# Kernel tuning notes

Hardware: AMD Instinct MI355X
Metric: run time of the kernel (lower is better)

## Reference

```python
import jax, jax.numpy as jnp
import numpy as np

HEAD = 12  # number of attention heads (init kwarg)


def setup_inputs() -> dict:
    key = jax.random.key(0)
    ks = jax.random.split(key, 6)
    B, N, F = 16, 1024, 768
    return {
        "x": jax.random.normal(ks[0], (B, N, F), dtype=jnp.float32),
        "wq": jax.random.normal(ks[1], (F,), dtype=jnp.float32),
        "bq": jnp.zeros((F,), dtype=jnp.float32),
        "wk": jax.random.normal(ks[2], (F,), dtype=jnp.float32),
        "bk": jnp.zeros((F,), dtype=jnp.float32),
        "wv": jax.random.normal(ks[3], (F,), dtype=jnp.float32),
        "bv": jnp.zeros((F,), dtype=jnp.float32),
        "wo": jax.random.normal(ks[4], (F,), dtype=jnp.float32),
        "bo": jnp.zeros((F,), dtype=jnp.float32),
    }


def reference(x, wq, bq, wk, bk, wv, bv, wo, bo):
    # x: [B, N, F]; depthwise (per-channel) q/k/v projections, MHSA, depthwise out proj
    B, N, F = x.shape
    d = F // HEAD
    scale = jnp.asarray(F, x.dtype) ** 0.5  # repo uses sqrt(feats), not sqrt(d_head)

    def to_heads(t):
        return t.reshape(B, N, HEAD, d)

    q = to_heads(x * wq + bq)  # [B, N, H, d]
    k = to_heads(x * wk + bk)
    v = to_heads(x * wv + bv)

    att = jnp.einsum("bqhd,bkhd->bhqk", q, k) / scale  # [B, H, N, N]
    att = jax.nn.softmax(att, axis=-1)
    o = jnp.einsum("bhqk,bkhd->bqhd", att, v).reshape(B, N, F)
    return o * wo + bo
```

## Files before the change

### kernel.cpp

```cpp
#include <hip/hip_runtime.h>
#include <hip/hip_bf16.h>
#include <cstdint>
#include <cstddef>

typedef __attribute__((ext_vector_type(8))) short short8;
typedef __attribute__((ext_vector_type(4))) short short4v;
typedef __attribute__((ext_vector_type(4))) float f32x4;
typedef __attribute__((ext_vector_type(16))) float f32x16;
typedef __attribute__((ext_vector_type(4))) unsigned int uint4v;

static constexpr int B_ = 16, N_ = 1024, F_ = 768, H_ = 12, D_ = 64;
static constexpr int NB = 64, NT = N_ / NB;
static constexpr int QB = 128;
static constexpr float RSCALE = 0.036084391824351615f;
static constexpr float QSCALE = 0.036084391824351615f * 1.4426950408889634f;
static constexpr float DEFER_THR = 8.0f;

__device__ __forceinline__ short f2bf(float f) {
    return __builtin_bit_cast(short, __float2bfloat16(f));
}
__device__ __forceinline__ unsigned cvtpk(float lo, float hi) {
    unsigned r;
    asm("v_cvt_pk_bf16_f32 %0, %1, %2" : "=v"(r) : "v"(lo), "v"(hi));
    return r;
}

#define GLB(p)  ((const __attribute__((address_space(1))) void*)(p))
#define LDSP(p) ((__attribute__((address_space(3))) void*)(p))

__global__ void __launch_bounds__(256) prep_kv(
    const float* __restrict__ x,
    const float* __restrict__ wk, const float* __restrict__ bk,
    const float* __restrict__ wv, const float* __restrict__ bv,
    short* __restrict__ Kt, short* __restrict__ Vt)
{
    const int bid = blockIdx.x;
    const int t   = bid & 15;
    const int bh  = bid >> 4;
    const int h   = bh % H_, b = bh / H_;
    const int nb  = t * NB;
    const int tid = threadIdx.x;
    short* Ktile = Kt + ((size_t)bid << 12);
    short* Vtile = Vt + ((size_t)bid << 12);

    {
        const int n = tid >> 2, sg = tid & 3;
        const float* xr  = x  + ((size_t)(b * N_ + nb + n)) * F_ + h * D_ + sg * 16;
        const float* wkp = wk + h * D_ + sg * 16;
        const float* bkp = bk + h * D_ + sg * 16;
        float xv[16];
        #pragma unroll
        for (int q = 0; q < 4; ++q) *(float4*)&xv[q * 4] = *(const float4*)(xr + q * 4);
        short kb[16];
        #pragma unroll
        for (int i = 0; i < 16; ++i) kb[i] = f2bf(xv[i] * wkp[i] + bkp[i]);
        const int swz = n & 7;
        #pragma unroll
        for (int c2 = 0; c2 < 2; ++c2) {
            const int c = sg * 2 + c2;
            *(short8*)&Ktile[n * 64 + ((c ^ swz) << 3)] = *(short8*)&kb[c2 * 8];
        }
    }
    {
        const int d = tid & 63, ng = tid >> 6;
        const float wvd = wv[h * D_ + d], bvd = bv[h * D_ + d];
        const float* xc = x + ((size_t)(b * N_ + nb + ng * 16)) * F_ + h * D_ + d;
        short vb[16];
        #pragma unroll
        for (int j = 0; j < 16; ++j) vb[j] = f2bf(xc[(size_t)j * F_] * wvd + bvd);
        const int swz = d & 7;
        #pragma unroll
        for (int c2 = 0; c2 < 2; ++c2) {
            const int c = ng * 2 + c2;
            *(short8*)&Vtile[d * 64 + ((c ^ swz) << 3)] = *(short8*)&vb[c2 * 8];
        }
    }
}

__global__ void __launch_bounds__(256, 4) attn_main(
    const float* __restrict__ x,
    const float* __restrict__ wq, const float* __restrict__ bq,
    const short* __restrict__ Kt, const short* __restrict__ Vt,
    const float* __restrict__ wo, const float* __restrict__ bo,
    float* __restrict__ out)
{
    __shared__ short KV[2][2][4096];

    const int tid  = threadIdx.x;
    const int w    = tid >> 6, lane = tid & 63;
    const int q32  = lane & 31, hi = lane >> 5;

    const int orig = blockIdx.x;
    const int sb   = (orig & 7) * 192 + (orig >> 3);
    const int qt   = sb & 7, bh = sb >> 3;
    const int h    = bh % H_, b = bh / H_;
    const int qrow0 = qt * QB + w * 32;
    const int qa    = qrow0 + q32;

    short8 qf[4];
    {
        const float* xq = x + ((size_t)(b * N_ + qa)) * F_ + h * D_;
        #pragma unroll
        for (int s = 0; s < 4; ++s) {
            const int ch0 = s * 16 + hi * 8;
            float4 a0 = *(const float4*)(xq + ch0);
            float4 a1 = *(const float4*)(xq + ch0 + 4);
            const float* wqp = wq + h * D_ + ch0;
            const float* bqp = bq + h * D_ + ch0;
            float q8[8] = {a0.x,a0.y,a0.z,a0.w,a1.x,a1.y,a1.z,a1.w};
            uint4v u;
            #pragma unroll
            for (int j = 0; j < 4; ++j) {
                const float lo = (q8[2*j]   * wqp[2*j]   + bqp[2*j])   * QSCALE;
                const float hf = (q8[2*j+1] * wqp[2*j+1] + bqp[2*j+1]) * QSCALE;
                u[j] = cvtpk(lo, hf);
            }
            qf[s] = __builtin_bit_cast(short8, u);
        }
    }

    const int swz = q32 & 7;
    int coff[4];
    #pragma unroll
    for (int s = 0; s < 4; ++s) coff[s] = (((s * 2 + hi) ^ swz) << 3);
    const int rA = q32 * 64;
    const int rB = (32 + q32) * 64;

    float m_ = 0.f, l_ = 0.f;
    f32x16 oA, oB;
    #pragma unroll
    for (int r = 0; r < 16; ++r) { oA[r] = 0.f; oB[r] = 0.f; }

    const size_t base = ((size_t)bh) * (NT * 4096);
    auto stage = [&](int buf, int tt) {
        const short* tk = Kt + base + ((size_t)tt << 12) + w * 1024 + (lane << 3);
        const short* tv = Vt + base + ((size_t)tt << 12) + w * 1024 + (lane << 3);
        __builtin_amdgcn_global_load_lds(GLB(tk),       LDSP(&KV[buf][0][w*1024]),       16, 0, 0);
        __builtin_amdgcn_global_load_lds(GLB(tk + 512), LDSP(&KV[buf][0][w*1024 + 512]), 16, 0, 0);
        __builtin_amdgcn_global_load_lds(GLB(tv),       LDSP(&KV[buf][1][w*1024]),       16, 0, 0);
        __builtin_amdgcn_global_load_lds(GLB(tv + 512), LDSP(&KV[buf][1][w*1024 + 512]), 16, 0, 0);
    };

    stage(0, 0);

    for (int t = 0; t < NT; ++t) {
        const int cur = t & 1;
        __syncthreads();
        if (t + 1 < NT) stage(cur ^ 1, t + 1);
        const short* Kb = &KV[cur][0][0];
        const short* Vb = &KV[cur][1][0];

        const float negm = -m_;
        f32x16 sA, sB;
        #pragma unroll
        for (int r = 0; r < 16; ++r) { sA[r] = negm; sB[r] = negm; }
        __builtin_amdgcn_s_setprio(1);
        #pragma unroll
        for (int s = 0; s < 4; ++s) {
            short8 k0 = *(const short8*)&Kb[rA + coff[s]];
            short8 k1 = *(const short8*)&Kb[rB + coff[s]];
            sA = __builtin_amdgcn_mfma_f32_32x32x16_bf16(k0, qf[s], sA, 0, 0, 0);
            sB = __builtin_amdgcn_mfma_f32_32x32x16_bf16(k1, qf[s], sB, 0, 0, 0);
        }
        __builtin_amdgcn_s_setprio(0);

        float mx[16];
        #pragma unroll
        for (int r = 0; r < 16; ++r) mx[r] = fmaxf(sA[r], sB[r]);
        #pragma unroll
        for (int off = 8; off > 0; off >>= 1) {
            #pragma unroll
            for (int i = 0; i < 8; ++i)
                if (i < off) mx[i] = fmaxf(mx[i], mx[i + off]);
        }
        const float tm = fmaxf(mx[0], __shfl_xor(mx[0], 32, 64));

        if (!__all(tm <= DEFER_THR)) {
            const float corr = __builtin_amdgcn_exp2f(-tm);
            l_ *= corr;
            #pragma unroll
            for (int r = 0; r < 16; ++r) { oA[r] *= corr; oB[r] *= corr; }
            #pragma unroll
            for (int r = 0; r < 16; ++r) { sA[r] -= tm; sB[r] -= tm; }
            m_ += tm;
        }

        float e[32];
        #pragma unroll
        for (int r = 0; r < 16; ++r) {
            e[r]      = __builtin_amdgcn_exp2f(sA[r]);
            e[16 + r] = __builtin_amdgcn_exp2f(sB[r]);
        }
        float su[16];
        #pragma unroll
        for (int i = 0; i < 16; ++i) su[i] = e[i] + e[i + 16];
        #pragma unroll
        for (int off = 8; off > 0; off >>= 1) {
            #pragma unroll
            for (int i = 0; i < 8; ++i)
                if (i < off) su[i] += su[i + off];
        }
        l_ += su[0] + __shfl_xor(su[0], 32, 64);

        short8 pf[4];
        {
            uint4v u0, u1, u2, u3;
            u0[0] = cvtpk(e[0],  e[1]);  u0[1] = cvtpk(e[2],  e[3]);
            u0[2] = cvtpk(e[4],  e[5]);  u0[3] = cvtpk(e[6],  e[7]);
            u1[0] = cvtpk(e[8],  e[9]);  u1[1] = cvtpk(e[10], e[11]);
            u1[2] = cvtpk(e[12], e[13]); u1[3] = cvtpk(e[14], e[15]);
            u2[0] = cvtpk(e[16], e[17]); u2[1] = cvtpk(e[18], e[19]);
            u2[2] = cvtpk(e[20], e[21]); u2[3] = cvtpk(e[22], e[23]);
            u3[0] = cvtpk(e[24], e[25]); u3[1] = cvtpk(e[26], e[27]);
            u3[2] = cvtpk(e[28], e[29]); u3[3] = cvtpk(e[30], e[31]);
            pf[0] = __builtin_bit_cast(short8, u0);
            pf[1] = __builtin_bit_cast(short8, u1);
            pf[2] = __builtin_bit_cast(short8, u2);
            pf[3] = __builtin_bit_cast(short8, u3);
        }

        __builtin_amdgcn_s_setprio(1);
        #pragma unroll
        for (int s = 0; s < 4; ++s) {
            const int cLo = ((2*s    ) ^ swz) << 3;
            const int cHi = ((2*s + 1) ^ swz) << 3;
            short4v aLo = *(const short4v*)&Vb[rA + cLo + 4*hi];
            short4v aHi = *(const short4v*)&Vb[rA + cHi + 4*hi];
            short4v bLo = *(const short4v*)&Vb[rB + cLo + 4*hi];
            short4v bHi = *(const short4v*)&Vb[rB + cHi + 4*hi];
            short8 v0 = {aLo[0],aLo[1],aLo[2],aLo[3], aHi[0],aHi[1],aHi[2],aHi[3]};
            short8 v1 = {bLo[0],bLo[1],bLo[2],bLo[3], bHi[0],bHi[1],bHi[2],bHi[3]};
            oA = __builtin_amdgcn_mfma_f32_32x32x16_bf16(v0, pf[s], oA, 0, 0, 0);
            oB = __builtin_amdgcn_mfma_f32_32x32x16_bf16(v1, pf[s], oB, 0, 0, 0);
        }
        __builtin_amdgcn_s_setprio(0);
    }

    const float invl = 1.f / l_;
    float* orow = out + ((size_t)(b * N_ + qa)) * F_;
    #pragma unroll
    for (int dsb = 0; dsb < 2; ++dsb) {
        #pragma unroll
        for (int j = 0; j < 4; ++j) {
            const int ch = h * D_ + dsb * 32 + 8 * j + 4 * hi;
            float4 wv = *(const float4*)(wo + ch);
            float4 bv = *(const float4*)(bo + ch);
            float4 o4;
            if (dsb == 0) {
                o4.x = oA[4*j+0] * invl * wv.x + bv.x;
                o4.y = oA[4*j+1] * invl * wv.y + bv.y;
                o4.z = oA[4*j+2] * invl * wv.z + bv.z;
                o4.w = oA[4*j+3] * invl * wv.w + bv.w;
            } else {
                o4.x = oB[4*j+0] * invl * wv.x + bv.x;
                o4.y = oB[4*j+1] * invl * wv.y + bv.y;
                o4.z = oB[4*j+2] * invl * wv.z + bv.z;
                o4.w = oB[4*j+3] * invl * wv.w + bv.w;
            }
            *(float4*)(orow + ch) = o4;
        }
    }
}

__global__ void __launch_bounds__(256) attn_fused(
    const float* __restrict__ x,
    const float* __restrict__ wq, const float* __restrict__ bq,
    const float* __restrict__ wk, const float* __restrict__ bk,
    const float* __restrict__ wv, const float* __restrict__ bv,
    const float* __restrict__ wo, const float* __restrict__ bo,
    float* __restrict__ out)
{
    __shared__ short Klds[64][72];
    __shared__ short Vt[64][72];
    __shared__ short Plds[4][16][72];

    const int tid = threadIdx.x;
    const int wave = tid >> 6, lane = tid & 63;
    const int g = lane >> 4, cc = lane & 15;
    const int bid = blockIdx.x;
    const int qt = bid & 15, t1 = bid >> 4;
    const int h = t1 % H_, b = t1 / H_;

    const int qrow = qt * 64 + wave * 16 + cc;
    const float* xq = x + ((size_t)(b * N_ + qrow)) * F_ + h * D_;
    short8 qf[2];
    #pragma unroll
    for (int kc = 0; kc < 2; ++kc) {
        const int dd = kc * 32 + g * 8;
        float4 a0 = *(const float4*)(xq + dd);
        float4 a1 = *(const float4*)(xq + dd + 4);
        float qa[8] = {a0.x,a0.y,a0.z,a0.w,a1.x,a1.y,a1.z,a1.w};
        #pragma unroll
        for (int i = 0; i < 8; ++i) {
            const int ch = h * D_ + dd + i;
            qf[kc][i] = f2bf((qa[i] * wq[ch] + bq[ch]) * RSCALE);
        }
    }
    const int srow = tid >> 2, seg = tid & 3;
    const int cb = h * D_ + seg * 16;
    float m_[4], l_[4];
    f32x4 oacc[4];
    #pragma unroll
    for (int r = 0; r < 4; ++r) { m_[r] = -INFINITY; l_[r] = 0.f; oacc[r] = (f32x4){0,0,0,0}; }

    for (int nb = 0; nb < N_; nb += 64) {
        __syncthreads();
        {
            const float* xr = x + ((size_t)(b * N_ + nb + srow)) * F_ + cb;
            float4 x0 = *(const float4*)(xr + 0), x1 = *(const float4*)(xr + 4);
            float4 x2 = *(const float4*)(xr + 8), x3 = *(const float4*)(xr + 12);
            float xf[16] = {x0.x,x0.y,x0.z,x0.w,x1.x,x1.y,x1.z,x1.w,
                            x2.x,x2.y,x2.z,x2.w,x3.x,x3.y,x3.z,x3.w};
            short8 k0, k1;
            #pragma unroll
            for (int i = 0; i < 8; ++i) {
                k0[i] = f2bf(xf[i] * wk[cb+i] + bk[cb+i]);
                k1[i] = f2bf(xf[i+8] * wk[cb+i+8] + bk[cb+i+8]);
            }
            *(short8*)&Klds[srow][seg*16] = k0;
            *(short8*)&Klds[srow][seg*16+8] = k1;
            #pragma unroll
            for (int i = 0; i < 16; ++i)
                Vt[seg*16+i][srow] = f2bf(xf[i] * wv[cb+i] + bv[cb+i]);
        }
        __syncthreads();
        f32x4 s[4];
        #pragma unroll
        for (int sub = 0; sub < 4; ++sub) {
            f32x4 acc = (f32x4){0,0,0,0};
            #pragma unroll
            for (int kc = 0; kc < 2; ++kc) {
                short8 kf = *(short8*)&Klds[sub*16+cc][kc*32+g*8];
                acc = __builtin_amdgcn_mfma_f32_16x16x32_bf16(qf[kc], kf, acc, 0,0,0);
            }
            s[sub] = acc;
        }
        float tm[4];
        #pragma unroll
        for (int r = 0; r < 4; ++r)
            tm[r] = fmaxf(fmaxf(s[0][r], s[1][r]), fmaxf(s[2][r], s[3][r]));
        #pragma unroll
        for (int r = 0; r < 4; ++r)
            #pragma unroll
            for (int off = 1; off < 16; off <<= 1)
                tm[r] = fmaxf(tm[r], __shfl_xor(tm[r], off, 64));
        float corr[4], ps[4];
        #pragma unroll
        for (int r = 0; r < 4; ++r) {
            float mn = fmaxf(m_[r], tm[r]);
            corr[r] = __expf(m_[r] - mn);
            m_[r] = mn; ps[r] = 0.f;
        }
        #pragma unroll
        for (int sub = 0; sub < 4; ++sub)
            #pragma unroll
            for (int r = 0; r < 4; ++r) {
                float p = __expf(s[sub][r] - m_[r]);
                s[sub][r] = p; ps[r] += p;
            }
        #pragma unroll
        for (int r = 0; r < 4; ++r) {
            #pragma unroll
            for (int off = 1; off < 16; off <<= 1)
                ps[r] += __shfl_xor(ps[r], off, 64);
            l_[r] = l_[r] * corr[r] + ps[r];
        }
        #pragma unroll
        for (int d = 0; d < 4; ++d)
            #pragma unroll
            for (int r = 0; r < 4; ++r) oacc[d][r] *= corr[r];
        #pragma unroll
        for (int sub = 0; sub < 4; ++sub)
            #pragma unroll
            for (int r = 0; r < 4; ++r)
                Plds[wave][g*4+r][sub*16+cc] = f2bf(s[sub][r]);
        short8 pf[2];
        #pragma unroll
        for (int nc = 0; nc < 2; ++nc)
            pf[nc] = *(short8*)&Plds[wave][cc][nc*32+g*8];
        #pragma unroll
        for (int d = 0; d < 4; ++d)
            #pragma unroll
            for (int nc = 0; nc < 2; ++nc) {
                short8 vf = *(short8*)&Vt[d*16+cc][nc*32+g*8];
                oacc[d] = __builtin_amdgcn_mfma_f32_16x16x32_bf16(pf[nc], vf, oacc[d], 0,0,0);
            }
    }
    #pragma unroll
    for (int r = 0; r < 4; ++r) l_[r] = 1.f / l_[r];
    const int orow0 = qt * 64 + wave * 16 + g * 4;
    #pragma unroll
    for (int d = 0; d < 4; ++d) {
        const int ch = h * D_ + d * 16 + cc;
        const float wov = wo[ch], bov = bo[ch];
        #pragma unroll
        for (int r = 0; r < 4; ++r)
            out[((size_t)(b * N_ + orow0 + r)) * F_ + ch] = oacc[d][r] * l_[r] * wov + bov;
    }
}

extern "C" void kernel_launch(void* const* d_in, const int* in_sizes, int n_in,
                              void* d_out, int out_size, void* d_ws, size_t ws_size,
                              hipStream_t stream) {
    const float* x  = (const float*)d_in[0];
    const float* wq = (const float*)d_in[1];
    const float* bq = (const float*)d_in[2];
    const float* wk = (const float*)d_in[3];
    const float* bk = (const float*)d_in[4];
    const float* wv = (const float*)d_in[5];
    const float* bv = (const float*)d_in[6];
    const float* wo = (const float*)d_in[7];
    const float* bo = (const float*)d_in[8];
    float* out = (float*)d_out;

    const size_t elems = (size_t)B_ * H_ * N_ * D_;
    const size_t need  = elems * 2 * 2;
    if (ws_size >= need) {
        short* Ktw = (short*)d_ws;
        short* Vtw = Ktw + elems;
        prep_kv<<<dim3(B_ * H_ * NT), dim3(256), 0, stream>>>(x, wk, bk, wv, bv, Ktw, Vtw);
        attn_main<<<dim3(B_ * H_ * (N_ / QB)), dim3(256), 0, stream>>>(
            x, wq, bq, Ktw, Vtw, wo, bo, out);
    } else {
        attn_fused<<<dim3(B_ * H_ * (N_ / 64)), dim3(256), 0, stream>>>(
            x, wq, bq, wk, bk, wv, bv, wo, bo, out);
    }
}
```

Before: 101.1 us.

## Split softmax into two half-tiles and pre-permute V tile for single short8 loads

Changes the V tile layout written by the prep kernel so each PV-MFMA operand can be fetched with one short8 LDS load, replacing the two short4 loads plus register shuffle per operand. Splits the per-tile online softmax into two 32-key halves, each with its own max, rescale, exp and sum, and issues the PV MFMAs for the first half before the second half's softmax so matrix and vector work can overlap. Also removes the s_setprio hints. The cost is a second max/shuffle reduction and a possible second rescale of the accumulators per tile.

```diff
diff --git a/kernel.cpp b/kernel.cpp
--- a/kernel.cpp
+++ b/kernel.cpp
@@ -4,7 +4,6 @@
 #include <cstddef>
 
 typedef __attribute__((ext_vector_type(8))) short short8;
-typedef __attribute__((ext_vector_type(4))) short short4v;
 typedef __attribute__((ext_vector_type(4))) float f32x4;
 typedef __attribute__((ext_vector_type(16))) float f32x16;
 typedef __attribute__((ext_vector_type(4))) unsigned int uint4v;
@@ -69,11 +68,10 @@
         #pragma unroll
         for (int j = 0; j < 16; ++j) vb[j] = f2bf(xc[(size_t)j * F_] * wvd + bvd);
         const int swz = d & 7;
-        #pragma unroll
-        for (int c2 = 0; c2 < 2; ++c2) {
-            const int c = ng * 2 + c2;
-            *(short8*)&Vtile[d * 64 + ((c ^ swz) << 3)] = *(short8*)&vb[c2 * 8];
-        }
+        short8 c0 = {vb[0], vb[1], vb[2],  vb[3],  vb[8],  vb[9],  vb[10], vb[11]};
+        short8 c1 = {vb[4], vb[5], vb[6],  vb[7],  vb[12], vb[13], vb[14], vb[15]};
+        *(short8*)&Vtile[d * 64 + (((ng * 2    ) ^ swz) << 3)] = c0;
+        *(short8*)&Vtile[d * 64 + (((ng * 2 + 1) ^ swz) << 3)] = c1;
     }
 }
 
@@ -154,7 +152,6 @@
         f32x16 sA, sB;
         #pragma unroll
         for (int r = 0; r < 16; ++r) { sA[r] = negm; sB[r] = negm; }
-        __builtin_amdgcn_s_setprio(1);
         #pragma unroll
         for (int s = 0; s < 4; ++s) {
             short8 k0 = *(const short8*)&Kb[rA + coff[s]];
@@ -162,78 +159,104 @@
             sA = __builtin_amdgcn_mfma_f32_32x32x16_bf16(k0, qf[s], sA, 0, 0, 0);
             sB = __builtin_amdgcn_mfma_f32_32x32x16_bf16(k1, qf[s], sB, 0, 0, 0);
         }
-        __builtin_amdgcn_s_setprio(0);
-
-        float mx[16];
-        #pragma unroll
-        for (int r = 0; r < 16; ++r) mx[r] = fmaxf(sA[r], sB[r]);
-        #pragma unroll
-        for (int off = 8; off > 0; off >>= 1) {
-            #pragma unroll
-            for (int i = 0; i < 8; ++i)
-                if (i < off) mx[i] = fmaxf(mx[i], mx[i + off]);
-        }
-        const float tm = fmaxf(mx[0], __shfl_xor(mx[0], 32, 64));
-
-        if (!__all(tm <= DEFER_THR)) {
-            const float corr = __builtin_amdgcn_exp2f(-tm);
-            l_ *= corr;
-            #pragma unroll
-            for (int r = 0; r < 16; ++r) { oA[r] *= corr; oB[r] *= corr; }
-            #pragma unroll
-            for (int r = 0; r < 16; ++r) { sA[r] -= tm; sB[r] -= tm; }
-            m_ += tm;
-        }
-
-        float e[32];
-        #pragma unroll
-        for (int r = 0; r < 16; ++r) {
-            e[r]      = __builtin_amdgcn_exp2f(sA[r]);
-            e[16 + r] = __builtin_amdgcn_exp2f(sB[r]);
-        }
-        float su[16];
-        #pragma unroll
-        for (int i = 0; i < 16; ++i) su[i] = e[i] + e[i + 16];
-        #pragma unroll
-        for (int off = 8; off > 0; off >>= 1) {
-            #pragma unroll
-            for (int i = 0; i < 8; ++i)
-                if (i < off) su[i] += su[i + off];
-        }
-        l_ += su[0] + __shfl_xor(su[0], 32, 64);
-
-        short8 pf[4];
+
         {
-            uint4v u0, u1, u2, u3;
-            u0[0] = cvtpk(e[0],  e[1]);  u0[1] = cvtpk(e[2],  e[3]);
-            u0[2] = cvtpk(e[4],  e[5]);  u0[3] = cvtpk(e[6],  e[7]);
-            u1[0] = cvtpk(e[8],  e[9]);  u1[1] = cvtpk(e[10], e[11]);
-            u1[2] = cvtpk(e[12], e[13]); u1[3] = cvtpk(e[14], e[15]);
-            u2[0] = cvtpk(e[16], e[17]); u2[1] = cvtpk(e[18], e[19]);
-            u2[2] = cvtpk(e[20], e[21]); u2[3] = cvtpk(e[22], e[23]);
-            u3[0] = cvtpk(e[24], e[25]); u3[1] = cvtpk(e[26], e[27]);
-            u3[2] = cvtpk(e[28], e[29]); u3[3] = cvtpk(e[30], e[31]);
-            pf[0] = __builtin_bit_cast(short8, u0);
-            pf[1] = __builtin_bit_cast(short8, u1);
-            pf[2] = __builtin_bit_cast(short8, u2);
-            pf[3] = __builtin_bit_cast(short8, u3);
-        }
-
-        __builtin_amdgcn_s_setprio(1);
-        #pragma unroll
-        for (int s = 0; s < 4; ++s) {
-            const int cLo = ((2*s    ) ^ swz) << 3;
-            const int cHi = ((2*s + 1) ^ swz) << 3;
-            short4v aLo = *(const short4v*)&Vb[rA + cLo + 4*hi];
-            short4v aHi = *(const short4v*)&Vb[rA + cHi + 4*hi];
-            short4v bLo = *(const short4v*)&Vb[rB + cLo + 4*hi];
-            short4v bHi = *(const short4v*)&Vb[rB + cHi + 4*hi];
-            short8 v0 = {aLo[0],aLo[1],aLo[2],aLo[3], aHi[0],aHi[1],aHi[2],aHi[3]};
-            short8 v1 = {bLo[0],bLo[1],bLo[2],bLo[3], bHi[0],bHi[1],bHi[2],bHi[3]};
-            oA = __builtin_amdgcn_mfma_f32_32x32x16_bf16(v0, pf[s], oA, 0, 0, 0);
-            oB = __builtin_amdgcn_mfma_f32_32x32x16_bf16(v1, pf[s], oB, 0, 0, 0);
-        }
-        __builtin_amdgcn_s_setprio(0);
+            float mx[8];
+            #pragma unroll
+            for (int i = 0; i < 8; ++i) mx[i] = fmaxf(sA[i], sA[i + 8]);
+            #pragma unroll
+            for (int off = 4; off > 0; off >>= 1)
+                #pragma unroll
+                for (int i = 0; i < 4; ++i)
+                    if (i < off) mx[i] = fmaxf(mx[i], mx[i + off]);
+            const float tmA = fmaxf(mx[0], __shfl_xor(mx[0], 32, 64));
+            if (!__all(tmA <= DEFER_THR)) {
+                const float corr = __builtin_amdgcn_exp2f(-tmA);
+                l_ *= corr;
+                #pragma unroll
+                for (int r = 0; r < 16; ++r) { oA[r] *= corr; oB[r] *= corr; }
+                #pragma unroll
+                for (int r = 0; r < 16; ++r) { sA[r] -= tmA; sB[r] -= tmA; }
+                m_ += tmA;
+            }
+            #pragma unroll
+            for (int r = 0; r < 16; ++r) sA[r] = __builtin_amdgcn_exp2f(sA[r]);
+            float su[8];
+            #pragma unroll
+            for (int i = 0; i < 8; ++i) su[i] = sA[i] + sA[i + 8];
+            #pragma unroll
+            for (int off = 4; off > 0; off >>= 1)
+                #pragma unroll
+                for (int i = 0; i < 4; ++i)
+                    if (i < off) su[i] += su[i + off];
+            l_ += su[0] + __shfl_xor(su[0], 32, 64);
+        }
+        short8 pfA[2];
+        {
+            uint4v u0, u1;
+            u0[0] = cvtpk(sA[0],  sA[1]);  u0[1] = cvtpk(sA[2],  sA[3]);
+            u0[2] = cvtpk(sA[4],  sA[5]);  u0[3] = cvtpk(sA[6],  sA[7]);
+            u1[0] = cvtpk(sA[8],  sA[9]);  u1[1] = cvtpk(sA[10], sA[11]);
+            u1[2] = cvtpk(sA[12], sA[13]); u1[3] = cvtpk(sA[14], sA[15]);
+            pfA[0] = __builtin_bit_cast(short8, u0);
+            pfA[1] = __builtin_bit_cast(short8, u1);
+        }
+        #pragma unroll
+        for (int s = 0; s < 2; ++s) {
+            short8 v0 = *(const short8*)&Vb[rA + coff[s]];
+            short8 v1 = *(const short8*)&Vb[rB + coff[s]];
+            oA = __builtin_amdgcn_mfma_f32_32x32x16_bf16(v0, pfA[s], oA, 0, 0, 0);
+            oB = __builtin_amdgcn_mfma_f32_32x32x16_bf16(v1, pfA[s], oB, 0, 0, 0);
+        }
+
+        {
+            float mx[8];
+            #pragma unroll
+            for (int i = 0; i < 8; ++i) mx[i] = fmaxf(sB[i], sB[i + 8]);
+            #pragma unroll
+            for (int off = 4; off > 0; off >>= 1)
+                #pragma unroll
+                for (int i = 0; i < 4; ++i)
+                    if (i < off) mx[i] = fmaxf(mx[i], mx[i + off]);
+            const float tmB = fmaxf(mx[0], __shfl_xor(mx[0], 32, 64));
+            if (!__all(tmB <= DEFER_THR)) {
+                const float corr = __builtin_amdgcn_exp2f(-tmB);
+                l_ *= corr;
+                #pragma unroll
+                for (int r = 0; r < 16; ++r) { oA[r] *= corr; oB[r] *= corr; }
+                #pragma unroll
+                for (int r = 0; r < 16; ++r) sB[r] -= tmB;
+                m_ += tmB;
+            }
+            #pragma unroll
+            for (int r = 0; r < 16; ++r) sB[r] = __builtin_amdgcn_exp2f(sB[r]);
+            float su[8];
+            #pragma unroll
+            for (int i = 0; i < 8; ++i) su[i] = sB[i] + sB[i + 8];
+            #pragma unroll
+            for (int off = 4; off > 0; off >>= 1)
+                #pragma unroll
+                for (int i = 0; i < 4; ++i)
+                    if (i < off) su[i] += su[i + off];
+            l_ += su[0] + __shfl_xor(su[0], 32, 64);
+        }
+        short8 pfB[2];
+        {
+            uint4v u2, u3;
+            u2[0] = cvtpk(sB[0],  sB[1]);  u2[1] = cvtpk(sB[2],  sB[3]);
+            u2[2] = cvtpk(sB[4],  sB[5]);  u2[3] = cvtpk(sB[6],  sB[7]);
+            u3[0] = cvtpk(sB[8],  sB[9]);  u3[1] = cvtpk(sB[10], sB[11]);
+            u3[2] = cvtpk(sB[12], sB[13]); u3[3] = cvtpk(sB[14], sB[15]);
+            pfB[0] = __builtin_bit_cast(short8, u2);
+            pfB[1] = __builtin_bit_cast(short8, u3);
+        }
+        #pragma unroll
+        for (int s = 2; s < 4; ++s) {
+            short8 v0 = *(const short8*)&Vb[rA + coff[s]];
+            short8 v1 = *(const short8*)&Vb[rB + coff[s]];
+            oA = __builtin_amdgcn_mfma_f32_32x32x16_bf16(v0, pfB[s - 2], oA, 0, 0, 0);
+            oB = __builtin_amdgcn_mfma_f32_32x32x16_bf16(v1, pfB[s - 2], oB, 0, 0, 0);
+        }
     }
 
     const float invl = 1.f / l_;
```

Result: faster. 96.41 us (median of 3 runs) (-4.7%).
